# Kernel optimization log

Hardware: AMD Instinct MI355X
Metric: run time of the kernel (lower is better)

Reference implementation:

```python
import jax, jax.numpy as jnp
import numpy as np


def setup_inputs() -> dict:
    key = jax.random.key(0)
    kx, ku, kf = jax.random.split(key, 3)
    N, F = 1024, 128
    x = jax.random.normal(kx, (N, F), dtype=jnp.float32)
    U = jax.random.normal(ku, (N, N), dtype=jnp.float32)
    # torch init makes each filter diagonal; replicate that structure
    stdv = 1.0 / np.sqrt(N)
    diag_vals = jax.random.uniform(kf, (F, N), minval=-stdv, maxval=stdv, dtype=jnp.float32)
    filters = jax.vmap(jnp.diag)(diag_vals)  # (F, N, N)
    return {"x": x, "U": U, "filters": filters}


def reference(x, U, filters):
    # Original per-filter math: out[i] = (U @ filters[i]) @ (U^T @ x[:, i])
    # Reassociated (same math): out[i] = U @ (filters[i] @ (U^T @ x[:, i]))
    y = U.T @ x                               # (N, F)
    z = jnp.einsum('fnm,mf->fn', filters, y)  # per-filter matvec, (F, N)
    out = jnp.einsum('nm,fm->fn', U, z)       # (F, N)
    return out
```

## Files before the change

### kernel.cpp

```cpp
#include <hip/hip_runtime.h>
#include <hip/hip_bf16.h>

#define NN 1024
#define FF 128
#define NSPLIT 8


__global__ __launch_bounds__(256) void gemm1(const float* __restrict__ U,
                                             const float* __restrict__ x,
                                             float* __restrict__ zp) {
    __shared__ float As[16][32];
    __shared__ float Bs[16][128];

    const int tid = threadIdx.x;
    const int tm = tid & 15;
    const int tf = tid >> 4;
    const int m0 = blockIdx.x * 32;
    const int s  = blockIdx.y;
    const int n0 = s * 128;

    float acc[2][8];
#pragma unroll
    for (int i = 0; i < 2; ++i)
#pragma unroll
        for (int j = 0; j < 8; ++j) acc[i][j] = 0.f;

    const int ka = tid >> 4, ma = (tid & 15) * 2;
    const int kb = tid >> 5, fb = (tid & 31) * 4;

    for (int kt = 0; kt < 8; ++kt) {
        const int nb = n0 + kt * 16;
        *(float2*)&As[ka][ma] = *(const float2*)&U[(size_t)(nb + ka) * NN + m0 + ma];
        *(float4*)&Bs[kb][fb]     = *(const float4*)&x[(size_t)(nb + kb) * FF + fb];
        *(float4*)&Bs[kb + 8][fb] = *(const float4*)&x[(size_t)(nb + kb + 8) * FF + fb];
        __syncthreads();
#pragma unroll
        for (int k = 0; k < 16; ++k) {
            const float2 a  = *(const float2*)&As[k][tm * 2];
            const float4 b0 = *(const float4*)&Bs[k][tf * 8];
            const float4 b1 = *(const float4*)&Bs[k][tf * 8 + 4];
            acc[0][0] += a.x * b0.x; acc[0][1] += a.x * b0.y;
            acc[0][2] += a.x * b0.z; acc[0][3] += a.x * b0.w;
            acc[0][4] += a.x * b1.x; acc[0][5] += a.x * b1.y;
            acc[0][6] += a.x * b1.z; acc[0][7] += a.x * b1.w;
            acc[1][0] += a.y * b0.x; acc[1][1] += a.y * b0.y;
            acc[1][2] += a.y * b0.z; acc[1][3] += a.y * b0.w;
            acc[1][4] += a.y * b1.x; acc[1][5] += a.y * b1.y;
            acc[1][6] += a.y * b1.z; acc[1][7] += a.y * b1.w;
        }
        __syncthreads();
    }

#pragma unroll
    for (int i = 0; i < 2; ++i) {
        const int m = m0 + tm * 2 + i;
#pragma unroll
        for (int j = 0; j < 8; ++j) {
            const int f = tf * 8 + j;
            zp[((size_t)s * FF + f) * NN + m] = acc[i][j];
        }
    }
}

__global__ __launch_bounds__(256) void reduce_scale(const float* __restrict__ filters,
                                                    const float* __restrict__ zp,
                                                    float* __restrict__ zt) {
    const int idx = blockIdx.x * 256 + threadIdx.x;
    const int f = idx >> 10;
    const int m = idx & 1023;
    float s = 0.f;
#pragma unroll
    for (int sp = 0; sp < NSPLIT; ++sp)
        s += zp[((size_t)sp * FF + f) * NN + m];
    const float d = filters[(size_t)f * (NN * NN) + (size_t)m * (NN + 1)];
    zt[(size_t)m * FF + f] = s * d;
}

__global__ __launch_bounds__(256) void gemm2(const float* __restrict__ U,
                                             const float* __restrict__ zt,
                                             float* __restrict__ op) {
    __shared__ float As[16][34];
    __shared__ float Bs[16][128];

    const int tid = threadIdx.x;
    const int tn = tid & 15;
    const int tf = tid >> 4;
    const int n0 = blockIdx.x * 32;
    const int s  = blockIdx.y;
    const int m0 = s * 128;

    float acc[2][8];
#pragma unroll
    for (int i = 0; i < 2; ++i)
#pragma unroll
        for (int j = 0; j < 8; ++j) acc[i][j] = 0.f;

    const int na = tid >> 3, kk = (tid & 7) * 2;
    const int kb = tid >> 5, fb = (tid & 31) * 4;

    for (int kt = 0; kt < 8; ++kt) {
        const int mb = m0 + kt * 16;
        const float2 v = *(const float2*)&U[(size_t)(n0 + na) * NN + mb + kk];
        As[kk][na]     = v.x;
        As[kk + 1][na] = v.y;
        *(float4*)&Bs[kb][fb]     = *(const float4*)&zt[(size_t)(mb + kb) * FF + fb];
        *(float4*)&Bs[kb + 8][fb] = *(const float4*)&zt[(size_t)(mb + kb + 8) * FF + fb];
        __syncthreads();
#pragma unroll
        for (int k = 0; k < 16; ++k) {
            const float2 a  = *(const float2*)&As[k][tn * 2];
            const float4 b0 = *(const float4*)&Bs[k][tf * 8];
            const float4 b1 = *(const float4*)&Bs[k][tf * 8 + 4];
            acc[0][0] += a.x * b0.x; acc[0][1] += a.x * b0.y;
            acc[0][2] += a.x * b0.z; acc[0][3] += a.x * b0.w;
            acc[0][4] += a.x * b1.x; acc[0][5] += a.x * b1.y;
            acc[0][6] += a.x * b1.z; acc[0][7] += a.x * b1.w;
            acc[1][0] += a.y * b0.x; acc[1][1] += a.y * b0.y;
            acc[1][2] += a.y * b0.z; acc[1][3] += a.y * b0.w;
            acc[1][4] += a.y * b1.x; acc[1][5] += a.y * b1.y;
            acc[1][6] += a.y * b1.z; acc[1][7] += a.y * b1.w;
        }
        __syncthreads();
    }

#pragma unroll
    for (int i = 0; i < 2; ++i) {
        const int n = n0 + tn * 2 + i;
#pragma unroll
        for (int j = 0; j < 8; ++j) {
            const int f = tf * 8 + j;
            op[((size_t)s * FF + f) * NN + n] = acc[i][j];
        }
    }
}

__global__ __launch_bounds__(256) void reduce_out(const float* __restrict__ op,
                                                  float* __restrict__ out) {
    const int idx = blockIdx.x * 256 + threadIdx.x;
    float s = 0.f;
#pragma unroll
    for (int sp = 0; sp < NSPLIT; ++sp)
        s += op[(size_t)sp * FF * NN + idx];
    out[idx] = s;
}

extern "C" void kernel_launch(void* const* d_in, const int* in_sizes, int n_in,
                              void* d_out, int out_size, void* d_ws, size_t ws_size,
                              hipStream_t stream) {
    const float* x       = (const float*)d_in[0];
    const float* U       = (const float*)d_in[1];
    const float* filters = (const float*)d_in[2];

    float* out = (float*)d_out;
    float* zp  = (float*)d_ws;
    float* zt  = zp + (size_t)NSPLIT * FF * NN;
    float* op  = zt + (size_t)NN * FF;

    gemm1<<<dim3(32, 8), 256, 0, stream>>>(U, x, zp);
    reduce_scale<<<dim3((NN * FF) / 256), 256, 0, stream>>>(filters, zp, zt);
    gemm2<<<dim3(32, 8), 256, 0, stream>>>(U, zt, op);
    reduce_out<<<dim3((NN * FF) / 256), 256, 0, stream>>>(op, out);
}
```

Measured before the change: 597.6 us.

## Fuse four stages into one cooperative kernel with grid-wide syncs

Merges the two split-K GEMMs and their reduction kernels into a single cooperative launch of 256 blocks, separated by grid.sync barriers. The reduction phases now process two elements per thread. This removes three kernel launch boundaries and their idle gaps. In exchange it adds grid-wide barrier costs and depends on all 256 blocks being co-resident.

```diff
diff --git a/kernel.cpp b/kernel.cpp
--- a/kernel.cpp
+++ b/kernel.cpp
@@ -1,147 +1,159 @@
 #include <hip/hip_runtime.h>
 #include <hip/hip_bf16.h>
+#include <hip/hip_cooperative_groups.h>
+
+namespace cg = cooperative_groups;
 
 #define NN 1024
 #define FF 128
 #define NSPLIT 8
 
+__global__ __launch_bounds__(256) void fused_gcl(const float* __restrict__ U,
+                                                 const float* __restrict__ x,
+                                                 const float* __restrict__ filters,
+                                                 float* __restrict__ zp,
+                                                 float* __restrict__ zt,
+                                                 float* __restrict__ op,
+                                                 float* __restrict__ out) {
+    cg::grid_group grid = cg::this_grid();
 
-__global__ __launch_bounds__(256) void gemm1(const float* __restrict__ U,
-                                             const float* __restrict__ x,
-                                             float* __restrict__ zp) {
-    __shared__ float As[16][32];
-    __shared__ float Bs[16][128];
-
-    const int tid = threadIdx.x;
-    const int tm = tid & 15;
-    const int tf = tid >> 4;
-    const int m0 = blockIdx.x * 32;
-    const int s  = blockIdx.y;
-    const int n0 = s * 128;
-
-    float acc[2][8];
-#pragma unroll
-    for (int i = 0; i < 2; ++i)
-#pragma unroll
-        for (int j = 0; j < 8; ++j) acc[i][j] = 0.f;
-
-    const int ka = tid >> 4, ma = (tid & 15) * 2;
-    const int kb = tid >> 5, fb = (tid & 31) * 4;
-
-    for (int kt = 0; kt < 8; ++kt) {
-        const int nb = n0 + kt * 16;
-        *(float2*)&As[ka][ma] = *(const float2*)&U[(size_t)(nb + ka) * NN + m0 + ma];
-        *(float4*)&Bs[kb][fb]     = *(const float4*)&x[(size_t)(nb + kb) * FF + fb];
-        *(float4*)&Bs[kb + 8][fb] = *(const float4*)&x[(size_t)(nb + kb + 8) * FF + fb];
-        __syncthreads();
-#pragma unroll
-        for (int k = 0; k < 16; ++k) {
-            const float2 a  = *(const float2*)&As[k][tm * 2];
-            const float4 b0 = *(const float4*)&Bs[k][tf * 8];
-            const float4 b1 = *(const float4*)&Bs[k][tf * 8 + 4];
-            acc[0][0] += a.x * b0.x; acc[0][1] += a.x * b0.y;
-            acc[0][2] += a.x * b0.z; acc[0][3] += a.x * b0.w;
-            acc[0][4] += a.x * b1.x; acc[0][5] += a.x * b1.y;
-            acc[0][6] += a.x * b1.z; acc[0][7] += a.x * b1.w;
-            acc[1][0] += a.y * b0.x; acc[1][1] += a.y * b0.y;
-            acc[1][2] += a.y * b0.z; acc[1][3] += a.y * b0.w;
-            acc[1][4] += a.y * b1.x; acc[1][5] += a.y * b1.y;
-            acc[1][6] += a.y * b1.z; acc[1][7] += a.y * b1.w;
-        }
-        __syncthreads();
-    }
-
-#pragma unroll
-    for (int i = 0; i < 2; ++i) {
-        const int m = m0 + tm * 2 + i;
-#pragma unroll
-        for (int j = 0; j < 8; ++j) {
-            const int f = tf * 8 + j;
-            zp[((size_t)s * FF + f) * NN + m] = acc[i][j];
-        }
-    }
-}
-
-__global__ __launch_bounds__(256) void reduce_scale(const float* __restrict__ filters,
-                                                    const float* __restrict__ zp,
-                                                    float* __restrict__ zt) {
-    const int idx = blockIdx.x * 256 + threadIdx.x;
-    const int f = idx >> 10;
-    const int m = idx & 1023;
-    float s = 0.f;
-#pragma unroll
-    for (int sp = 0; sp < NSPLIT; ++sp)
-        s += zp[((size_t)sp * FF + f) * NN + m];
-    const float d = filters[(size_t)f * (NN * NN) + (size_t)m * (NN + 1)];
-    zt[(size_t)m * FF + f] = s * d;
-}
-
-__global__ __launch_bounds__(256) void gemm2(const float* __restrict__ U,
-                                             const float* __restrict__ zt,
-                                             float* __restrict__ op) {
     __shared__ float As[16][34];
     __shared__ float Bs[16][128];
 
     const int tid = threadIdx.x;
-    const int tn = tid & 15;
-    const int tf = tid >> 4;
-    const int n0 = blockIdx.x * 32;
-    const int s  = blockIdx.y;
-    const int m0 = s * 128;
+    const int bid = blockIdx.x;
 
-    float acc[2][8];
+    {
+        const int tm = tid & 15;
+        const int tf = tid >> 4;
+        const int m0 = (bid & 31) * 32;
+        const int s  = bid >> 5;
+        const int n0 = s * 128;
+
+        float acc[2][8];
 #pragma unroll
-    for (int i = 0; i < 2; ++i)
+        for (int i = 0; i < 2; ++i)
 #pragma unroll
-        for (int j = 0; j < 8; ++j) acc[i][j] = 0.f;
+            for (int j = 0; j < 8; ++j) acc[i][j] = 0.f;
 
-    const int na = tid >> 3, kk = (tid & 7) * 2;
-    const int kb = tid >> 5, fb = (tid & 31) * 4;
+        const int ka = tid >> 4, ma = (tid & 15) * 2;
+        const int kb = tid >> 5, fb = (tid & 31) * 4;
 
-    for (int kt = 0; kt < 8; ++kt) {
-        const int mb = m0 + kt * 16;
-        const float2 v = *(const float2*)&U[(size_t)(n0 + na) * NN + mb + kk];
-        As[kk][na]     = v.x;
-        As[kk + 1][na] = v.y;
-        *(float4*)&Bs[kb][fb]     = *(const float4*)&zt[(size_t)(mb + kb) * FF + fb];
-        *(float4*)&Bs[kb + 8][fb] = *(const float4*)&zt[(size_t)(mb + kb + 8) * FF + fb];
-        __syncthreads();
+        for (int kt = 0; kt < 8; ++kt) {
+            const int nb = n0 + kt * 16;
+            *(float2*)&As[ka][ma] = *(const float2*)&U[(size_t)(nb + ka) * NN + m0 + ma];
+            *(float4*)&Bs[kb][fb]     = *(const float4*)&x[(size_t)(nb + kb) * FF + fb];
+            *(float4*)&Bs[kb + 8][fb] = *(const float4*)&x[(size_t)(nb + kb + 8) * FF + fb];
+            __syncthreads();
 #pragma unroll
-        for (int k = 0; k < 16; ++k) {
-            const float2 a  = *(const float2*)&As[k][tn * 2];
-            const float4 b0 = *(const float4*)&Bs[k][tf * 8];
-            const float4 b1 = *(const float4*)&Bs[k][tf * 8 + 4];
-            acc[0][0] += a.x * b0.x; acc[0][1] += a.x * b0.y;
-            acc[0][2] += a.x * b0.z; acc[0][3] += a.x * b0.w;
-            acc[0][4] += a.x * b1.x; acc[0][5] += a.x * b1.y;
-            acc[0][6] += a.x * b1.z; acc[0][7] += a.x * b1.w;
-            acc[1][0] += a.y * b0.x; acc[1][1] += a.y * b0.y;
-            acc[1][2] += a.y * b0.z; acc[1][3] += a.y * b0.w;
-            acc[1][4] += a.y * b1.x; acc[1][5] += a.y * b1.y;
-            acc[1][6] += a.y * b1.z; acc[1][7] += a.y * b1.w;
+            for (int k = 0; k < 16; ++k) {
+                const float2 a  = *(const float2*)&As[k][tm * 2];
+                const float4 b0 = *(const float4*)&Bs[k][tf * 8];
+                const float4 b1 = *(const float4*)&Bs[k][tf * 8 + 4];
+                acc[0][0] += a.x * b0.x; acc[0][1] += a.x * b0.y;
+                acc[0][2] += a.x * b0.z; acc[0][3] += a.x * b0.w;
+                acc[0][4] += a.x * b1.x; acc[0][5] += a.x * b1.y;
+                acc[0][6] += a.x * b1.z; acc[0][7] += a.x * b1.w;
+                acc[1][0] += a.y * b0.x; acc[1][1] += a.y * b0.y;
+                acc[1][2] += a.y * b0.z; acc[1][3] += a.y * b0.w;
+                acc[1][4] += a.y * b1.x; acc[1][5] += a.y * b1.y;
+                acc[1][6] += a.y * b1.z; acc[1][7] += a.y * b1.w;
+            }
+            __syncthreads();
         }
-        __syncthreads();
-    }
 
 #pragma unroll
-    for (int i = 0; i < 2; ++i) {
-        const int n = n0 + tn * 2 + i;
+        for (int i = 0; i < 2; ++i) {
+            const int m = m0 + tm * 2 + i;
 #pragma unroll
-        for (int j = 0; j < 8; ++j) {
-            const int f = tf * 8 + j;
-            op[((size_t)s * FF + f) * NN + n] = acc[i][j];
+            for (int j = 0; j < 8; ++j) {
+                const int f = tf * 8 + j;
+                zp[((size_t)s * FF + f) * NN + m] = acc[i][j];
+            }
         }
     }
-}
+    grid.sync();
 
-__global__ __launch_bounds__(256) void reduce_out(const float* __restrict__ op,
-                                                  float* __restrict__ out) {
-    const int idx = blockIdx.x * 256 + threadIdx.x;
-    float s = 0.f;
+    {
 #pragma unroll
-    for (int sp = 0; sp < NSPLIT; ++sp)
-        s += op[(size_t)sp * FF * NN + idx];
-    out[idx] = s;
+        for (int r = 0; r < 2; ++r) {
+            const int idx = bid * 512 + r * 256 + tid;
+            const int f = idx >> 10;
+            const int m = idx & 1023;
+            float s = 0.f;
+#pragma unroll
+            for (int sp = 0; sp < NSPLIT; ++sp)
+                s += zp[((size_t)sp * FF + f) * NN + m];
+            const float d = filters[(size_t)f * (NN * NN) + (size_t)m * (NN + 1)];
+            zt[(size_t)m * FF + f] = s * d;
+        }
+    }
+    grid.sync();
+
+    {
+        const int tn = tid & 15;
+        const int tf = tid >> 4;
+        const int n0 = (bid & 31) * 32;
+        const int s  = bid >> 5;
+        const int m0 = s * 128;
+
+        float acc[2][8];
+#pragma unroll
+        for (int i = 0; i < 2; ++i)
+#pragma unroll
+            for (int j = 0; j < 8; ++j) acc[i][j] = 0.f;
+
+        const int na = tid >> 3, kk = (tid & 7) * 2;
+        const int kb = tid >> 5, fb = (tid & 31) * 4;
+
+        for (int kt = 0; kt < 8; ++kt) {
+            const int mb = m0 + kt * 16;
+            const float2 v = *(const float2*)&U[(size_t)(n0 + na) * NN + mb + kk];
+            As[kk][na]     = v.x;
+            As[kk + 1][na] = v.y;
+            *(float4*)&Bs[kb][fb]     = *(const float4*)&zt[(size_t)(mb + kb) * FF + fb];
+            *(float4*)&Bs[kb + 8][fb] = *(const float4*)&zt[(size_t)(mb + kb + 8) * FF + fb];
+            __syncthreads();
+#pragma unroll
+            for (int k = 0; k < 16; ++k) {
+                const float2 a  = *(const float2*)&As[k][tn * 2];
+                const float4 b0 = *(const float4*)&Bs[k][tf * 8];
+                const float4 b1 = *(const float4*)&Bs[k][tf * 8 + 4];
+                acc[0][0] += a.x * b0.x; acc[0][1] += a.x * b0.y;
+                acc[0][2] += a.x * b0.z; acc[0][3] += a.x * b0.w;
+                acc[0][4] += a.x * b1.x; acc[0][5] += a.x * b1.y;
+                acc[0][6] += a.x * b1.z; acc[0][7] += a.x * b1.w;
+                acc[1][0] += a.y * b0.x; acc[1][1] += a.y * b0.y;
+                acc[1][2] += a.y * b0.z; acc[1][3] += a.y * b0.w;
+                acc[1][4] += a.y * b1.x; acc[1][5] += a.y * b1.y;
+                acc[1][6] += a.y * b1.z; acc[1][7] += a.y * b1.w;
+            }
+            __syncthreads();
+        }
+
+#pragma unroll
+        for (int i = 0; i < 2; ++i) {
+            const int n = n0 + tn * 2 + i;
+#pragma unroll
+            for (int j = 0; j < 8; ++j) {
+                const int f = tf * 8 + j;
+                op[((size_t)s * FF + f) * NN + n] = acc[i][j];
+            }
+        }
+    }
+    grid.sync();
+
+    {
+#pragma unroll
+        for (int r = 0; r < 2; ++r) {
+            const int idx = bid * 512 + r * 256 + tid;
+            float s = 0.f;
+#pragma unroll
+            for (int sp = 0; sp < NSPLIT; ++sp)
+                s += op[(size_t)sp * FF * NN + idx];
+            out[idx] = s;
+        }
+    }
 }
 
 extern "C" void kernel_launch(void* const* d_in, const int* in_sizes, int n_in,
@@ -156,8 +168,8 @@
     float* zt  = zp + (size_t)NSPLIT * FF * NN;
     float* op  = zt + (size_t)NN * FF;
 
-    gemm1<<<dim3(32, 8), 256, 0, stream>>>(U, x, zp);
-    reduce_scale<<<dim3((NN * FF) / 256), 256, 0, stream>>>(filters, zp, zt);
-    gemm2<<<dim3(32, 8), 256, 0, stream>>>(U, zt, op);
-    reduce_out<<<dim3((NN * FF) / 256), 256, 0, stream>>>(op, out);
+    void* args[] = {(void*)&U, (void*)&x, (void*)&filters,
+                    (void*)&zp, (void*)&zt, (void*)&op, (void*)&out};
+    hipLaunchCooperativeKernel((const void*)fused_gcl, dim3(256), dim3(256),
+                               args, 0, stream);
 }
```

After: 699.3 us. 17.0% more time.
